# Optimization experiments

Measured on AMD Instinct MI355X. Metric: run time of the kernel, lower is better.

Reference implementation:

```python
import jax, jax.numpy as jnp
import numpy as np


def _projectors():
    """DeGrand-Rossi gamma matrices; returns (Pm_re, Pm_im, Pp_re, Pp_im), each (4,4,4) float32."""
    i = 1j
    g0 = np.array([[0, 0, 0, i], [0, 0, i, 0], [0, -i, 0, 0], [-i, 0, 0, 0]], dtype=np.complex64)
    g1 = np.array([[0, 0, 0, -1], [0, 0, 1, 0], [0, 1, 0, 0], [-1, 0, 0, 0]], dtype=np.complex64)
    g2 = np.array([[0, 0, i, 0], [0, 0, 0, -i], [-i, 0, 0, 0], [0, i, 0, 0]], dtype=np.complex64)
    g3 = np.array([[0, 0, 1, 0], [0, 0, 0, 1], [1, 0, 0, 0], [0, 1, 0, 0]], dtype=np.complex64)
    G = np.stack([g0, g1, g2, g3])  # (4, 4, 4)
    I4 = np.eye(4, dtype=np.complex64)
    Pm = I4[None] - G
    Pp = I4[None] + G
    return (jnp.asarray(Pm.real, jnp.float32), jnp.asarray(Pm.imag, jnp.float32),
            jnp.asarray(Pp.real, jnp.float32), jnp.asarray(Pp.imag, jnp.float32))


def setup_inputs() -> dict:
    key = jax.random.key(0)
    k1, k2, k3, k4 = jax.random.split(key, 4)
    L = (32, 32, 32, 32)  # lattice volume
    psi_shape = L + (4, 3)      # (lattice..., spin, color)
    U_shape = L + (4, 3, 3)     # (lattice..., mu, color, color)
    psi_re = jax.random.normal(k1, psi_shape, jnp.float32)
    psi_im = jax.random.normal(k2, psi_shape, jnp.float32)
    U_re = jax.random.normal(k3, U_shape, jnp.float32)
    U_im = jax.random.normal(k4, U_shape, jnp.float32)
    Pm_re, Pm_im, Pp_re, Pp_im = _projectors()
    return {"psi_re": psi_re, "psi_im": psi_im, "U_re": U_re, "U_im": U_im,
            "Pm_re": Pm_re, "Pm_im": Pm_im, "Pp_re": Pp_re, "Pp_im": Pp_im}


def _color_mv(Ur, Ui, vr, vi):
    # U @ v per spin: (...,3,3) x (...,4,3) -> (...,4,3)
    rr = jnp.einsum('...ij,...sj->...si', Ur, vr) - jnp.einsum('...ij,...sj->...si', Ui, vi)
    ri = jnp.einsum('...ij,...sj->...si', Ur, vi) + jnp.einsum('...ij,...sj->...si', Ui, vr)
    return rr, ri


def _color_dag_mv(Ur, Ui, vr, vi):
    # U^dagger @ v per spin
    rr = jnp.einsum('...ji,...sj->...si', Ur, vr) + jnp.einsum('...ji,...sj->...si', Ui, vi)
    ri = jnp.einsum('...ji,...sj->...si', Ur, vi) - jnp.einsum('...ji,...sj->...si', Ui, vr)
    return rr, ri


def _spin_mv(Pr, Pi, vr, vi):
    # P @ v: (4,4) x (...,4,3) -> (...,4,3)
    rr = jnp.einsum('ij,...jk->...ik', Pr, vr) - jnp.einsum('ij,...jk->...ik', Pi, vi)
    ri = jnp.einsum('ij,...jk->...ik', Pr, vi) + jnp.einsum('ij,...jk->...ik', Pi, vr)
    return rr, ri


def reference(psi_re, psi_im, U_re, U_im, Pm_re, Pm_im, Pp_re, Pp_im):
    res_re = jnp.zeros_like(psi_re)
    res_im = jnp.zeros_like(psi_im)
    for mu in range(4):
        # psi has 6 dims, so dims=mu-6 in torch == axis mu here (same for 6-dim U_mu)
        Umr = U_re[..., mu, :, :]
        Umi = U_im[..., mu, :, :]
        # forward hop: P_minus U_mu(x) psi(x+mu)
        pf_re = jnp.roll(psi_re, -1, axis=mu)
        pf_im = jnp.roll(psi_im, -1, axis=mu)
        Upf_re, Upf_im = _color_mv(Umr, Umi, pf_re, pf_im)
        cf_re, cf_im = _spin_mv(Pm_re[mu], Pm_im[mu], Upf_re, Upf_im)
        # backward hop: P_plus U_mu^dagger(x-mu) psi(x-mu)
        pb_re = jnp.roll(psi_re, 1, axis=mu)
        pb_im = jnp.roll(psi_im, 1, axis=mu)
        Ub_re = jnp.roll(Umr, 1, axis=mu)
        Ub_im = jnp.roll(Umi, 1, axis=mu)
        Upb_re, Upb_im = _color_dag_mv(Ub_re, Ub_im, pb_re, pb_im)
        cb_re, cb_im = _spin_mv(Pp_re[mu], Pp_im[mu], Upb_re, Upb_im)
        res_re = res_re - 0.5 * (cf_re + cb_re)
        res_im = res_im - 0.5 * (cf_im + cb_im)
    return (res_re, res_im)
```

## Files before the change

kernel.cpp:

```cpp
#include <hip/hip_runtime.h>


static constexpr int SITES = 32 * 32 * 32 * 32;

__device__ __forceinline__ void load12(const float* __restrict__ p, float* v) {
    const float4* q = reinterpret_cast<const float4*>(p);
    float4 a = q[0], b = q[1], c = q[2];
    v[0] = a.x; v[1] = a.y; v[2]  = a.z; v[3]  = a.w;
    v[4] = b.x; v[5] = b.y; v[6]  = b.z; v[7]  = b.w;
    v[8] = c.x; v[9] = c.y; v[10] = c.z; v[11] = c.w;
}

__global__ __launch_bounds__(128) void wilson_dslash_kernel(
    const float* __restrict__ psi_re, const float* __restrict__ psi_im,
    const float* __restrict__ U_re,   const float* __restrict__ U_im,
    float* __restrict__ out_re,       float* __restrict__ out_im)
{
    const int blk  = ((blockIdx.x & 7) << 10) | (blockIdx.x >> 3);
    const int tid  = threadIdx.x;
    const int site = blk * 128 + tid;

    __shared__ float uf[128 * 76];
    float* myu = &uf[tid * 76];
    {
        const float4* pr = reinterpret_cast<const float4*>(U_re + (size_t)site * 36);
        const float4* pi = reinterpret_cast<const float4*>(U_im + (size_t)site * 36);
        float4* dr = reinterpret_cast<float4*>(myu);
        float4* di = reinterpret_cast<float4*>(myu + 40);
#pragma unroll
        for (int k = 0; k < 9; ++k) { dr[k] = pr[k]; di[k] = pi[k]; }
    }

    float ar[12], ai[12];
#pragma unroll
    for (int k = 0; k < 12; ++k) { ar[k] = 0.f; ai[k] = 0.f; }

#pragma unroll 1
    for (int mu = 0; mu < 4; ++mu) {
        const int sh  = 15 - 5 * mu;
        const int S   = 1 << sh;
        const int cmu = (site >> sh) & 31;
        const int nf  = site + (cmu == 31 ? -31 * S : S);
        const int nb  = site + (cmu == 0  ?  31 * S : -S);

        float vr[12], vi[12];
        float hr[6], hi[6];
        float gr[6], gi[6];

        load12(psi_re + (size_t)nf * 12, vr);
        load12(psi_im + (size_t)nf * 12, vi);
        const float* urp = myu + mu * 9;
        const float* uip = myu + 40 + mu * 9;
        if (mu == 0) {
#pragma unroll
            for (int c = 0; c < 3; ++c) {
                hr[c]     = vr[c]     + vi[9 + c];  hi[c]     = vi[c]     - vr[9 + c];
                hr[3 + c] = vr[3 + c] + vi[6 + c];  hi[3 + c] = vi[3 + c] - vr[6 + c];
            }
        } else if (mu == 1) {
#pragma unroll
            for (int c = 0; c < 3; ++c) {
                hr[c]     = vr[c]     + vr[9 + c];  hi[c]     = vi[c]     + vi[9 + c];
                hr[3 + c] = vr[3 + c] - vr[6 + c];  hi[3 + c] = vi[3 + c] - vi[6 + c];
            }
        } else if (mu == 2) {
#pragma unroll
            for (int c = 0; c < 3; ++c) {
                hr[c]     = vr[c]     + vi[6 + c];  hi[c]     = vi[c]     - vr[6 + c];
                hr[3 + c] = vr[3 + c] - vi[9 + c];  hi[3 + c] = vi[3 + c] + vr[9 + c];
            }
        } else {
#pragma unroll
            for (int c = 0; c < 3; ++c) {
                hr[c]     = vr[c]     - vr[6 + c];  hi[c]     = vi[c]     - vi[6 + c];
                hr[3 + c] = vr[3 + c] - vr[9 + c];  hi[3 + c] = vi[3 + c] - vi[9 + c];
            }
        }
#pragma unroll
        for (int s = 0; s < 2; ++s)
#pragma unroll
            for (int i = 0; i < 3; ++i) {
                float rr = 0.f, im = 0.f;
#pragma unroll
                for (int j = 0; j < 3; ++j) {
                    const float a = urp[i * 3 + j], b = uip[i * 3 + j];
                    rr += a * hr[s * 3 + j] - b * hi[s * 3 + j];
                    im += a * hi[s * 3 + j] + b * hr[s * 3 + j];
                }
                gr[s * 3 + i] = rr; gi[s * 3 + i] = im;
            }
#pragma unroll
        for (int c = 0; c < 3; ++c) {
            ar[c]     += gr[c];      ai[c]     += gi[c];
            ar[3 + c] += gr[3 + c];  ai[3 + c] += gi[3 + c];
        }
        if (mu == 0) {
#pragma unroll
            for (int c = 0; c < 3; ++c) {
                ar[6 + c] -= gi[3 + c];  ai[6 + c] += gr[3 + c];
                ar[9 + c] -= gi[c];      ai[9 + c] += gr[c];
            }
        } else if (mu == 1) {
#pragma unroll
            for (int c = 0; c < 3; ++c) {
                ar[6 + c] -= gr[3 + c];  ai[6 + c] -= gi[3 + c];
                ar[9 + c] += gr[c];      ai[9 + c] += gi[c];
            }
        } else if (mu == 2) {
#pragma unroll
            for (int c = 0; c < 3; ++c) {
                ar[6 + c] -= gi[c];      ai[6 + c] += gr[c];
                ar[9 + c] += gi[3 + c];  ai[9 + c] -= gr[3 + c];
            }
        } else {
#pragma unroll
            for (int c = 0; c < 3; ++c) {
                ar[6 + c] -= gr[c];      ai[6 + c] -= gi[c];
                ar[9 + c] -= gr[3 + c];  ai[9 + c] -= gi[3 + c];
            }
        }

        load12(psi_re + (size_t)nb * 12, vr);
        load12(psi_im + (size_t)nb * 12, vi);
        float ur[9], ui[9];
        {
            const float* pur = U_re + ((size_t)nb * 4 + mu) * 9;
            const float* pui = U_im + ((size_t)nb * 4 + mu) * 9;
#pragma unroll
            for (int k = 0; k < 9; ++k) { ur[k] = pur[k]; ui[k] = pui[k]; }
        }
        if (mu == 0) {
#pragma unroll
            for (int c = 0; c < 3; ++c) {
                hr[c]     = vr[c]     - vi[9 + c];  hi[c]     = vi[c]     + vr[9 + c];
                hr[3 + c] = vr[3 + c] - vi[6 + c];  hi[3 + c] = vi[3 + c] + vr[6 + c];
            }
        } else if (mu == 1) {
#pragma unroll
            for (int c = 0; c < 3; ++c) {
                hr[c]     = vr[c]     - vr[9 + c];  hi[c]     = vi[c]     - vi[9 + c];
                hr[3 + c] = vr[3 + c] + vr[6 + c];  hi[3 + c] = vi[3 + c] + vi[6 + c];
            }
        } else if (mu == 2) {
#pragma unroll
            for (int c = 0; c < 3; ++c) {
                hr[c]     = vr[c]     - vi[6 + c];  hi[c]     = vi[c]     + vr[6 + c];
                hr[3 + c] = vr[3 + c] + vi[9 + c];  hi[3 + c] = vi[3 + c] - vr[9 + c];
            }
        } else {
#pragma unroll
            for (int c = 0; c < 3; ++c) {
                hr[c]     = vr[c]     + vr[6 + c];  hi[c]     = vi[c]     + vi[6 + c];
                hr[3 + c] = vr[3 + c] + vr[9 + c];  hi[3 + c] = vi[3 + c] + vi[9 + c];
            }
        }
#pragma unroll
        for (int s = 0; s < 2; ++s)
#pragma unroll
            for (int i = 0; i < 3; ++i) {
                float rr = 0.f, im = 0.f;
#pragma unroll
                for (int j = 0; j < 3; ++j) {
                    rr += ur[j * 3 + i] * hr[s * 3 + j] + ui[j * 3 + i] * hi[s * 3 + j];
                    im += ur[j * 3 + i] * hi[s * 3 + j] - ui[j * 3 + i] * hr[s * 3 + j];
                }
                gr[s * 3 + i] = rr; gi[s * 3 + i] = im;
            }
#pragma unroll
        for (int c = 0; c < 3; ++c) {
            ar[c]     += gr[c];      ai[c]     += gi[c];
            ar[3 + c] += gr[3 + c];  ai[3 + c] += gi[3 + c];
        }
        if (mu == 0) {
#pragma unroll
            for (int c = 0; c < 3; ++c) {
                ar[6 + c] += gi[3 + c];  ai[6 + c] -= gr[3 + c];
                ar[9 + c] += gi[c];      ai[9 + c] -= gr[c];
            }
        } else if (mu == 1) {
#pragma unroll
            for (int c = 0; c < 3; ++c) {
                ar[6 + c] += gr[3 + c];  ai[6 + c] += gi[3 + c];
                ar[9 + c] -= gr[c];      ai[9 + c] -= gi[c];
            }
        } else if (mu == 2) {
#pragma unroll
            for (int c = 0; c < 3; ++c) {
                ar[6 + c] += gi[c];      ai[6 + c] -= gr[c];
                ar[9 + c] -= gi[3 + c];  ai[9 + c] += gr[3 + c];
            }
        } else {
#pragma unroll
            for (int c = 0; c < 3; ++c) {
                ar[6 + c] += gr[c];      ai[6 + c] += gi[c];
                ar[9 + c] += gr[3 + c];  ai[9 + c] += gi[3 + c];
            }
        }
    }

    float4* orp = reinterpret_cast<float4*>(out_re + (size_t)site * 12);
    float4* oip = reinterpret_cast<float4*>(out_im + (size_t)site * 12);
    orp[0] = make_float4(-0.5f * ar[0], -0.5f * ar[1], -0.5f * ar[2],  -0.5f * ar[3]);
    orp[1] = make_float4(-0.5f * ar[4], -0.5f * ar[5], -0.5f * ar[6],  -0.5f * ar[7]);
    orp[2] = make_float4(-0.5f * ar[8], -0.5f * ar[9], -0.5f * ar[10], -0.5f * ar[11]);
    oip[0] = make_float4(-0.5f * ai[0], -0.5f * ai[1], -0.5f * ai[2],  -0.5f * ai[3]);
    oip[1] = make_float4(-0.5f * ai[4], -0.5f * ai[5], -0.5f * ai[6],  -0.5f * ai[7]);
    oip[2] = make_float4(-0.5f * ai[8], -0.5f * ai[9], -0.5f * ai[10], -0.5f * ai[11]);
}

extern "C" void kernel_launch(void* const* d_in, const int* in_sizes, int n_in,
                              void* d_out, int out_size, void* d_ws, size_t ws_size,
                              hipStream_t stream) {
    const float* psi_re = (const float*)d_in[0];
    const float* psi_im = (const float*)d_in[1];
    const float* U_re   = (const float*)d_in[2];
    const float* U_im   = (const float*)d_in[3];
    float* out_re = (float*)d_out;
    float* out_im = out_re + (size_t)SITES * 12;

    wilson_dslash_kernel<<<SITES / 128, 128, 0, stream>>>(
        psi_re, psi_im, U_re, U_im, out_re, out_im);
}
```

Measured before the change: 538.0 us.

## Remap blocks to 2D x-y tiles per XCD and hoist mu=2,3 links into registers

Replaces the linear block-to-site mapping with one that gives each XCD a 16x8 tile in x-y, with blocks covering z-slabs, so neighbour psi and U reads in x and y are more likely to hit that XCD's L2. The mu=3 and mu=2 hops are peeled into compile-time specialised phases that use link matrices held in registers. Only mu=0,1 links go to a smaller padded shared-memory slot. The cost is higher register pressure, which can lower occupancy or cause spills.

```diff
diff --git a/kernel.cpp b/kernel.cpp
--- a/kernel.cpp
+++ b/kernel.cpp
@@ -11,84 +11,192 @@
     v[8] = c.x; v[9] = c.y; v[10] = c.z; v[11] = c.w;
 }
 
+__device__ __forceinline__ void mulU(const float* ur, const float* ui,
+                                     const float* hr, const float* hi,
+                                     float* gr, float* gi) {
+#pragma unroll
+    for (int s = 0; s < 2; ++s)
+#pragma unroll
+        for (int i = 0; i < 3; ++i) {
+            float rr = 0.f, im = 0.f;
+#pragma unroll
+            for (int j = 0; j < 3; ++j) {
+                const float a = ur[i * 3 + j], b = ui[i * 3 + j];
+                rr += a * hr[s * 3 + j] - b * hi[s * 3 + j];
+                im += a * hi[s * 3 + j] + b * hr[s * 3 + j];
+            }
+            gr[s * 3 + i] = rr; gi[s * 3 + i] = im;
+        }
+}
+
+__device__ __forceinline__ void mulUdag(const float* ur, const float* ui,
+                                        const float* hr, const float* hi,
+                                        float* gr, float* gi) {
+#pragma unroll
+    for (int s = 0; s < 2; ++s)
+#pragma unroll
+        for (int i = 0; i < 3; ++i) {
+            float rr = 0.f, im = 0.f;
+#pragma unroll
+            for (int j = 0; j < 3; ++j) {
+                const float a = ur[j * 3 + i], b = ui[j * 3 + i];
+                rr += a * hr[s * 3 + j] + b * hi[s * 3 + j];
+                im += a * hi[s * 3 + j] - b * hr[s * 3 + j];
+            }
+            gr[s * 3 + i] = rr; gi[s * 3 + i] = im;
+        }
+}
+
+template<int MU>
+__device__ __forceinline__ void phase_static(
+    int site,
+    const float* __restrict__ psi_re, const float* __restrict__ psi_im,
+    const float* __restrict__ U_re,   const float* __restrict__ U_im,
+    const float* ufr, const float* ufi,
+    float* ar, float* ai)
+{
+    const int sh  = 15 - 5 * MU;
+    const int S   = 1 << sh;
+    const int cmu = (site >> sh) & 31;
+    const int nf  = site + (cmu == 31 ? -31 * S : S);
+    const int nb  = site + (cmu == 0  ?  31 * S : -S);
+
+    float vr[12], vi[12], hr[6], hi[6], gr[6], gi[6];
+
+    load12(psi_re + (size_t)nf * 12, vr);
+    load12(psi_im + (size_t)nf * 12, vi);
+#pragma unroll
+    for (int c = 0; c < 3; ++c) {
+        if constexpr (MU == 2) {
+            hr[c]     = vr[c]     + vi[6 + c];  hi[c]     = vi[c]     - vr[6 + c];
+            hr[3 + c] = vr[3 + c] - vi[9 + c];  hi[3 + c] = vi[3 + c] + vr[9 + c];
+        } else {
+            hr[c]     = vr[c]     - vr[6 + c];  hi[c]     = vi[c]     - vi[6 + c];
+            hr[3 + c] = vr[3 + c] - vr[9 + c];  hi[3 + c] = vi[3 + c] - vi[9 + c];
+        }
+    }
+    mulU(ufr, ufi, hr, hi, gr, gi);
+#pragma unroll
+    for (int c = 0; c < 3; ++c) {
+        ar[c]     += gr[c];      ai[c]     += gi[c];
+        ar[3 + c] += gr[3 + c];  ai[3 + c] += gi[3 + c];
+        if constexpr (MU == 2) {
+            ar[6 + c] -= gi[c];      ai[6 + c] += gr[c];
+            ar[9 + c] += gi[3 + c];  ai[9 + c] -= gr[3 + c];
+        } else {
+            ar[6 + c] -= gr[c];      ai[6 + c] -= gi[c];
+            ar[9 + c] -= gr[3 + c];  ai[9 + c] -= gi[3 + c];
+        }
+    }
+
+    load12(psi_re + (size_t)nb * 12, vr);
+    load12(psi_im + (size_t)nb * 12, vi);
+    float ur[9], ui[9];
+    {
+        const float* pur = U_re + ((size_t)nb * 4 + MU) * 9;
+        const float* pui = U_im + ((size_t)nb * 4 + MU) * 9;
+#pragma unroll
+        for (int k = 0; k < 9; ++k) { ur[k] = pur[k]; ui[k] = pui[k]; }
+    }
+#pragma unroll
+    for (int c = 0; c < 3; ++c) {
+        if constexpr (MU == 2) {
+            hr[c]     = vr[c]     - vi[6 + c];  hi[c]     = vi[c]     + vr[6 + c];
+            hr[3 + c] = vr[3 + c] + vi[9 + c];  hi[3 + c] = vi[3 + c] - vr[9 + c];
+        } else {
+            hr[c]     = vr[c]     + vr[6 + c];  hi[c]     = vi[c]     + vi[6 + c];
+            hr[3 + c] = vr[3 + c] + vr[9 + c];  hi[3 + c] = vi[3 + c] + vi[9 + c];
+        }
+    }
+    mulUdag(ur, ui, hr, hi, gr, gi);
+#pragma unroll
+    for (int c = 0; c < 3; ++c) {
+        ar[c]     += gr[c];      ai[c]     += gi[c];
+        ar[3 + c] += gr[3 + c];  ai[3 + c] += gi[3 + c];
+        if constexpr (MU == 2) {
+            ar[6 + c] += gi[c];      ai[6 + c] -= gr[c];
+            ar[9 + c] -= gi[3 + c];  ai[9 + c] += gr[3 + c];
+        } else {
+            ar[6 + c] += gr[c];      ai[6 + c] += gi[c];
+            ar[9 + c] += gr[3 + c];  ai[9 + c] += gi[3 + c];
+        }
+    }
+}
+
 __global__ __launch_bounds__(128) void wilson_dslash_kernel(
     const float* __restrict__ psi_re, const float* __restrict__ psi_im,
     const float* __restrict__ U_re,   const float* __restrict__ U_im,
     float* __restrict__ out_re,       float* __restrict__ out_im)
 {
-    const int blk  = ((blockIdx.x & 7) << 10) | (blockIdx.x >> 3);
+    const int cxcd = blockIdx.x & 7;
+    const int r    = blockIdx.x >> 3;
+    const int xl   = r >> 6;
+    const int rem  = r & 63;
+    const int yl   = rem >> 3;
+    const int zq   = rem & 7;
+    const int x    = ((cxcd & 1) << 4) | xl;
+    const int y    = ((cxcd >> 1) << 3) | yl;
     const int tid  = threadIdx.x;
-    const int site = blk * 128 + tid;
-
-    __shared__ float uf[128 * 76];
-    float* myu = &uf[tid * 76];
+    const int site = (x << 15) | (y << 10) | (zq << 7) | tid;
+
+    __shared__ float uf[128 * 41];
+    float* slot = &uf[tid * 41];
+
+    float u2r[9], u2i[9], u3r[9], u3i[9];
     {
+        float fre[36], fim[36];
         const float4* pr = reinterpret_cast<const float4*>(U_re + (size_t)site * 36);
         const float4* pi = reinterpret_cast<const float4*>(U_im + (size_t)site * 36);
-        float4* dr = reinterpret_cast<float4*>(myu);
-        float4* di = reinterpret_cast<float4*>(myu + 40);
-#pragma unroll
-        for (int k = 0; k < 9; ++k) { dr[k] = pr[k]; di[k] = pi[k]; }
+#pragma unroll
+        for (int k = 0; k < 9; ++k) {
+            float4 a = pr[k], b = pi[k];
+            fre[4 * k + 0] = a.x; fre[4 * k + 1] = a.y; fre[4 * k + 2] = a.z; fre[4 * k + 3] = a.w;
+            fim[4 * k + 0] = b.x; fim[4 * k + 1] = b.y; fim[4 * k + 2] = b.z; fim[4 * k + 3] = b.w;
+        }
+#pragma unroll
+        for (int k = 0; k < 18; ++k) { slot[k] = fre[k]; slot[18 + k] = fim[k]; }
+#pragma unroll
+        for (int k = 0; k < 9; ++k) {
+            u2r[k] = fre[18 + k]; u2i[k] = fim[18 + k];
+            u3r[k] = fre[27 + k]; u3i[k] = fim[27 + k];
+        }
     }
 
     float ar[12], ai[12];
 #pragma unroll
     for (int k = 0; k < 12; ++k) { ar[k] = 0.f; ai[k] = 0.f; }
 
+    phase_static<3>(site, psi_re, psi_im, U_re, U_im, u3r, u3i, ar, ai);
+    phase_static<2>(site, psi_re, psi_im, U_re, U_im, u2r, u2i, ar, ai);
+
 #pragma unroll 1
-    for (int mu = 0; mu < 4; ++mu) {
+    for (int mu = 1; mu >= 0; --mu) {
         const int sh  = 15 - 5 * mu;
         const int S   = 1 << sh;
         const int cmu = (site >> sh) & 31;
         const int nf  = site + (cmu == 31 ? -31 * S : S);
         const int nb  = site + (cmu == 0  ?  31 * S : -S);
-
-        float vr[12], vi[12];
-        float hr[6], hi[6];
-        float gr[6], gi[6];
+        const float* ufr = slot + mu * 9;
+        const float* ufi = slot + 18 + mu * 9;
+
+        float vr[12], vi[12], hr[6], hi[6], gr[6], gi[6];
 
         load12(psi_re + (size_t)nf * 12, vr);
         load12(psi_im + (size_t)nf * 12, vi);
-        const float* urp = myu + mu * 9;
-        const float* uip = myu + 40 + mu * 9;
         if (mu == 0) {
 #pragma unroll
             for (int c = 0; c < 3; ++c) {
                 hr[c]     = vr[c]     + vi[9 + c];  hi[c]     = vi[c]     - vr[9 + c];
                 hr[3 + c] = vr[3 + c] + vi[6 + c];  hi[3 + c] = vi[3 + c] - vr[6 + c];
             }
-        } else if (mu == 1) {
+        } else {
 #pragma unroll
             for (int c = 0; c < 3; ++c) {
                 hr[c]     = vr[c]     + vr[9 + c];  hi[c]     = vi[c]     + vi[9 + c];
                 hr[3 + c] = vr[3 + c] - vr[6 + c];  hi[3 + c] = vi[3 + c] - vi[6 + c];
             }
-        } else if (mu == 2) {
-#pragma unroll
-            for (int c = 0; c < 3; ++c) {
-                hr[c]     = vr[c]     + vi[6 + c];  hi[c]     = vi[c]     - vr[6 + c];
-                hr[3 + c] = vr[3 + c] - vi[9 + c];  hi[3 + c] = vi[3 + c] + vr[9 + c];
-            }
-        } else {
-#pragma unroll
-            for (int c = 0; c < 3; ++c) {
-                hr[c]     = vr[c]     - vr[6 + c];  hi[c]     = vi[c]     - vi[6 + c];
-                hr[3 + c] = vr[3 + c] - vr[9 + c];  hi[3 + c] = vi[3 + c] - vi[9 + c];
-            }
-        }
-#pragma unroll
-        for (int s = 0; s < 2; ++s)
-#pragma unroll
-            for (int i = 0; i < 3; ++i) {
-                float rr = 0.f, im = 0.f;
-#pragma unroll
-                for (int j = 0; j < 3; ++j) {
-                    const float a = urp[i * 3 + j], b = uip[i * 3 + j];
-                    rr += a * hr[s * 3 + j] - b * hi[s * 3 + j];
-                    im += a * hi[s * 3 + j] + b * hr[s * 3 + j];
-                }
-                gr[s * 3 + i] = rr; gi[s * 3 + i] = im;
-            }
+        }
+        mulU(ufr, ufi, hr, hi, gr, gi);
 #pragma unroll
         for (int c = 0; c < 3; ++c) {
             ar[c]     += gr[c];      ai[c]     += gi[c];
@@ -100,23 +208,11 @@
                 ar[6 + c] -= gi[3 + c];  ai[6 + c] += gr[3 + c];
                 ar[9 + c] -= gi[c];      ai[9 + c] += gr[c];
             }
-        } else if (mu == 1) {
+        } else {
 #pragma unroll
             for (int c = 0; c < 3; ++c) {
                 ar[6 + c] -= gr[3 + c];  ai[6 + c] -= gi[3 + c];
                 ar[9 + c] += gr[c];      ai[9 + c] += gi[c];
-            }
-        } else if (mu == 2) {
-#pragma unroll
-            for (int c = 0; c < 3; ++c) {
-                ar[6 + c] -= gi[c];      ai[6 + c] += gr[c];
-                ar[9 + c] += gi[3 + c];  ai[9 + c] -= gr[3 + c];
-            }
-        } else {
-#pragma unroll
-            for (int c = 0; c < 3; ++c) {
-                ar[6 + c] -= gr[c];      ai[6 + c] -= gi[c];
-                ar[9 + c] -= gr[3 + c];  ai[9 + c] -= gi[3 + c];
             }
         }
 
@@ -135,37 +231,14 @@
                 hr[c]     = vr[c]     - vi[9 + c];  hi[c]     = vi[c]     + vr[9 + c];
                 hr[3 + c] = vr[3 + c] - vi[6 + c];  hi[3 + c] = vi[3 + c] + vr[6 + c];
             }
-        } else if (mu == 1) {
+        } else {
 #pragma unroll
             for (int c = 0; c < 3; ++c) {
                 hr[c]     = vr[c]     - vr[9 + c];  hi[c]     = vi[c]     - vi[9 + c];
                 hr[3 + c] = vr[3 + c] + vr[6 + c];  hi[3 + c] = vi[3 + c] + vi[6 + c];
             }
-        } else if (mu == 2) {
-#pragma unroll
-            for (int c = 0; c < 3; ++c) {
-                hr[c]     = vr[c]     - vi[6 + c];  hi[c]     = vi[c]     + vr[6 + c];
-                hr[3 + c] = vr[3 + c] + vi[9 + c];  hi[3 + c] = vi[3 + c] - vr[9 + c];
-            }
-        } else {
-#pragma unroll
-            for (int c = 0; c < 3; ++c) {
-                hr[c]     = vr[c]     + vr[6 + c];  hi[c]     = vi[c]     + vi[6 + c];
-                hr[3 + c] = vr[3 + c] + vr[9 + c];  hi[3 + c] = vi[3 + c] + vi[9 + c];
-            }
-        }
-#pragma unroll
-        for (int s = 0; s < 2; ++s)
-#pragma unroll
-            for (int i = 0; i < 3; ++i) {
-                float rr = 0.f, im = 0.f;
-#pragma unroll
-                for (int j = 0; j < 3; ++j) {
-                    rr += ur[j * 3 + i] * hr[s * 3 + j] + ui[j * 3 + i] * hi[s * 3 + j];
-                    im += ur[j * 3 + i] * hi[s * 3 + j] - ui[j * 3 + i] * hr[s * 3 + j];
-                }
-                gr[s * 3 + i] = rr; gi[s * 3 + i] = im;
-            }
+        }
+        mulUdag(ur, ui, hr, hi, gr, gi);
 #pragma unroll
         for (int c = 0; c < 3; ++c) {
             ar[c]     += gr[c];      ai[c]     += gi[c];
@@ -177,23 +250,11 @@
                 ar[6 + c] += gi[3 + c];  ai[6 + c] -= gr[3 + c];
                 ar[9 + c] += gi[c];      ai[9 + c] -= gr[c];
             }
-        } else if (mu == 1) {
+        } else {
 #pragma unroll
             for (int c = 0; c < 3; ++c) {
                 ar[6 + c] += gr[3 + c];  ai[6 + c] += gi[3 + c];
                 ar[9 + c] -= gr[c];      ai[9 + c] -= gi[c];
-            }
-        } else if (mu == 2) {
-#pragma unroll
-            for (int c = 0; c < 3; ++c) {
-                ar[6 + c] += gi[c];      ai[6 + c] -= gr[c];
-                ar[9 + c] -= gi[3 + c];  ai[9 + c] += gr[3 + c];
-            }
-        } else {
-#pragma unroll
-            for (int c = 0; c < 3; ++c) {
-                ar[6 + c] += gr[c];      ai[6 + c] += gi[c];
-                ar[9 + c] += gr[3 + c];  ai[9 + c] += gi[3 + c];
             }
         }
     }
```

Measured after the change: 555.9 us. 1.03x slower.
